# Performance work log

Measured on AMD Instinct MI355X. Metric: run time of the kernel, lower is better.

## Reference

```python
import jax, jax.numpy as jnp
import numpy as np

P = 10                      # half-window; kernel size K = 2P+1 = 21
GROUPS = ((0, 1000), (1000, 2000))  # hardcoded self.group = [0, 1000, 2000]


def setup_inputs() -> dict:
    key = jax.random.key(0)
    k1, k2, k3 = jax.random.split(key, 3)
    n, T, D = 16, 1024, 2000
    x = jax.random.normal(k1, (n, T, D), dtype=jnp.float32)
    W0 = jax.random.normal(k2, (D, 2 * P + 1), dtype=jnp.float32)
    W1 = jax.random.normal(k3, (D, 2 * P + 1), dtype=jnp.float32)
    return {"x": x, "W0": W0, "W1": W1}


def _shift_attention(x, Ws):
    n, T, D = x.shape
    K = 2 * P + 1
    # x_padded built from the ORIGINAL x under no_grad (detached)
    xp = jax.lax.stop_gradient(jnp.pad(x, ((0, 0), (P, P), (0, 0))))
    cur = x
    for Wi, (s, e) in zip(Ws, GROUPS):
        # dynamic per-timestep window weights: (n, T, K)
        w = jnp.einsum('ntd,dk->ntk', cur, Wi)
        xg = xp[:, :, s:e]  # (n, T+2P, g)
        # out[:, t, :] = sum_k w[:, t, k] * xg[:, t+k, :]  (windowed combine)
        out = w[:, :, 0, None] * xg[:, 0:T, :]
        for k in range(1, K):  # fixed small tap count, not a data-dim loop
            out = out + w[:, :, k, None] * xg[:, k:k + T, :]
        # in-place column update -> group 1 sees group 0's result in 'cur'
        cur = cur.at[:, :, s:e].set(out)
    return cur


def reference(x, W0, W1):
    return _shift_attention(x, (W0, W1))
```

## Files before the change

kernel.cpp:

```cpp
#include <hip/hip_runtime.h>

#define N_  16
#define T_  1024
#define D_  2000
#define K_  21
#define P_  10
#define NT_ (N_*T_)

__global__ void k_padW(const float* __restrict__ W0, const float* __restrict__ W1,
                       float* __restrict__ W0p, float* __restrict__ W1p) {
    int gid = blockIdx.x * blockDim.x + threadIdx.x;
    if (gid >= D_ * 24) return;
    int d = gid / 24, kk = gid - d * 24;
    W0p[gid] = (kk < K_) ? W0[d * K_ + kk] : 0.f;
    W1p[gid] = (kk < K_) ? W1[d * K_ + kk] : 0.f;
}

__global__ __launch_bounds__(256, 3)
void k_coef(const float* __restrict__ x,
            const float* __restrict__ W0p, const float* __restrict__ W1p,
            float* __restrict__ q0, float* __restrict__ q1,
            float* __restrict__ q2, float* __restrict__ q3,
            float* __restrict__ mp0, float* __restrict__ mp1,
            float* __restrict__ mp2, float* __restrict__ mp3) {
    __shared__ float lds[5888];
    const int tid  = threadIdx.x;
    const int lane = tid & 63;
    const int w    = __builtin_amdgcn_readfirstlane(tid >> 6);
    const int rg   = blockIdx.x >> 2;
    const int h    = blockIdx.x & 3;
    const int r0   = rg * 64;
    const int d0q  = h * 500;

    float a0[K_], a1[K_];
#pragma unroll
    for (int k = 0; k < K_; ++k) { a0[k] = 0.f; a1[k] = 0.f; }

    const int srow = tid >> 2;
    const int sf4  = (tid & 3) * 2;
    float4 ra, rb;

    auto load_tile = [&](int dt) {
        const int c0 = dt + sf4 * 4;
        const float* p = x + (size_t)(r0 + srow) * D_ + d0q + c0;
        ra = (c0 < 500)     ? *reinterpret_cast<const float4*>(p)
                            : make_float4(0.f, 0.f, 0.f, 0.f);
        rb = (c0 + 4 < 500) ? *reinterpret_cast<const float4*>(p + 4)
                            : make_float4(0.f, 0.f, 0.f, 0.f);
    };
    auto write_tile = [&](int buf) {
        float* b = lds + buf * 2112 + srow * 33 + sf4 * 4;
        b[0] = ra.x; b[1] = ra.y; b[2] = ra.z; b[3] = ra.w;
        b[4] = rb.x; b[5] = rb.y; b[6] = rb.z; b[7] = rb.w;
    };

    load_tile(0);
    write_tile(0);
    __syncthreads();

    for (int t = 0; t < 16; ++t) {
        if (t < 15) load_tile((t + 1) * 32);
        const int cw = (t < 15) ? 32 : 20;
        const float* xrow = lds + (t & 1) * 2112 + lane * 33;
#pragma unroll
        for (int c = 0; c < 8; ++c) {
            const int col = w * 8 + c;
            if (col < cw) {
                const int d = d0q + t * 32 + col;
                int duv;
                asm("v_mov_b32 %0, %1" : "=v"(duv) : "s"(d));
                const float* w0r = W0p + duv * 24;
                const float* w1r = W1p + duv * 24;
                float wa[21], wb[21];
#pragma unroll
                for (int j = 0; j < 5; ++j) {
                    *reinterpret_cast<float4*>(&wa[4 * j]) =
                        *reinterpret_cast<const float4*>(w0r + 4 * j);
                    *reinterpret_cast<float4*>(&wb[4 * j]) =
                        *reinterpret_cast<const float4*>(w1r + 4 * j);
                }
                wa[20] = w0r[20];
                wb[20] = w1r[20];
                const float xv = xrow[col];
#pragma unroll
                for (int k = 0; k < K_; ++k) a0[k] = fmaf(xv, wa[k], a0[k]);
#pragma unroll
                for (int k = 0; k < K_; ++k) a1[k] = fmaf(xv, wb[k], a1[k]);
            }
        }
        if (t < 15) write_tile((t + 1) & 1);
        __syncthreads();
    }

    auto reduce_store = [&](const float* acc, float* dst) {
        __syncthreads();
#pragma unroll
        for (int k = 0; k < K_; ++k) lds[tid * 23 + k] = acc[k];
        __syncthreads();
        for (int o = tid; o < 64 * K_; o += 256) {
            int tt = o / K_, j = o - tt * K_;
            float s = lds[tt * 23 + j] + lds[(64 + tt) * 23 + j] +
                      lds[(128 + tt) * 23 + j] + lds[(192 + tt) * 23 + j];
            dst[(size_t)(r0 + tt) * K_ + j] = s;
        }
    };

    float* const qd[4] = {q0, q1, q2, q3};
    float* const md[4] = {mp0, mp1, mp2, mp3};
    reduce_store(a0, qd[h]);
    reduce_store(a1, md[h]);
}

__global__ __launch_bounds__(256)
void k_finish(const float* __restrict__ q0, const float* __restrict__ q1,
              const float* __restrict__ q2, const float* __restrict__ q3,
              const float* __restrict__ mp0, const float* __restrict__ mp1,
              const float* __restrict__ mp2, const float* __restrict__ mp3,
              float* __restrict__ w0f, float* __restrict__ w1f) {
    __shared__ float w0s[64 * K_];
    __shared__ float Ms[84 * K_];
    const int tid = threadIdx.x;
    const int r0 = blockIdx.x * 64;

    for (int o = tid; o < 64 * K_; o += 256) {
        size_t g = (size_t)r0 * K_ + o;
        w0s[o] = q0[g] + q1[g] + q2[g] + q3[g];
    }
    for (int o = tid; o < 84 * K_; o += 256) {
        int i = o / K_, j = o - i * K_;
        int rr = r0 - P_ + i;
        float v = 0.f;
        if (rr >= 0 && rr < NT_) {
            size_t g = (size_t)rr * K_ + j;
            v = mp0[g] + mp1[g];
        }
        Ms[o] = v;
    }
    __syncthreads();

    for (int o = tid; o < 64 * K_; o += 256) {
        int row = o / K_, k = o - row * K_;
        size_t g = (size_t)(r0 + row) * K_ + k;
        float acc = mp2[g] + mp3[g];
        int t = (r0 + row) & (T_ - 1);
#pragma unroll
        for (int j = 0; j < K_; ++j) {
            int tt = t + j - P_;
            if (tt >= 0 && tt < T_)
                acc = fmaf(w0s[row * K_ + j], Ms[(row + j) * K_ + k], acc);
        }
        w1f[g] = acc;
        w0f[g] = w0s[o];
    }
}

__global__ __launch_bounds__(256)
void k_conv(const float* __restrict__ x, const float* __restrict__ w0f,
            const float* __restrict__ w1f, float* __restrict__ out) {
    __shared__ float xsl[84][128];
    __shared__ float wc[64 * 24];
    const int b = blockIdx.x;
    const int dseg = b & 7;
    const int tch  = (b >> 3) & 15;
    const int nn   = (b >> 7) & 15;
    const int grp  = b >> 11;
    const float* __restrict__ coef = grp ? w1f : w0f;
    const int dbase = grp * 1000;
    const int t0 = tch * 64;
    const int tid = threadIdx.x;
    const float* xb = x + (size_t)nn * T_ * D_;

    {
        const int scol = tid & 31, srow0 = tid >> 5;
#pragma unroll
        for (int pass = 0; pass < 11; ++pass) {
            int rr = srow0 + pass * 8;
            if (rr < 84) {
                int u = t0 - P_ + rr;
                int dl = dseg * 128 + scol * 4;
                float4 v = make_float4(0.f, 0.f, 0.f, 0.f);
                if (u >= 0 && u < T_ && dl < 1000)
                    v = *reinterpret_cast<const float4*>(xb + (size_t)u * D_ + dbase + dl);
                *reinterpret_cast<float4*>(&xsl[rr][scol * 4]) = v;
            }
        }
    }
    for (int o = tid; o < 64 * 24; o += 256) {
        int tl = o / 24, k = o - tl * 24;
        wc[o] = (k < K_) ? coef[((size_t)nn * T_ + t0 + tl) * K_ + k] : 0.f;
    }
    __syncthreads();

    const int wv = tid >> 6, lane = tid & 63;
    const int rw = wv * 16;
    const int dcol = dseg * 128 + lane * 2;
    const bool act = (dcol < 1000);

    float2 win[21];
#pragma unroll
    for (int s = 0; s < 21; ++s)
        win[s] = *reinterpret_cast<const float2*>(&xsl[rw + s][lane * 2]);

    float* obase = out + ((size_t)nn * T_ + t0 + rw) * D_ + dbase + dcol;

#pragma unroll
    for (int i = 0; i < 16; ++i) {
        float cfa[24];
        const float4* cf = reinterpret_cast<const float4*>(&wc[(rw + i) * 24]);
#pragma unroll
        for (int j = 0; j < 5; ++j)
            *reinterpret_cast<float4*>(&cfa[4 * j]) = cf[j];
        cfa[20] = wc[(rw + i) * 24 + 20];
        float2 acc = make_float2(0.f, 0.f);
#pragma unroll
        for (int k = 0; k < K_; ++k) {
            const float2 xv = win[(i + k) % 21];
            acc.x = fmaf(cfa[k], xv.x, acc.x);
            acc.y = fmaf(cfa[k], xv.y, acc.y);
        }
        if (act) *reinterpret_cast<float2*>(obase + (size_t)i * D_) = acc;
        if (i < 15)
            win[i % 21] = *reinterpret_cast<const float2*>(&xsl[rw + i + 21][lane * 2]);
    }
}

extern "C" void kernel_launch(void* const* d_in, const int* in_sizes, int n_in,
                              void* d_out, int out_size, void* d_ws, size_t ws_size,
                              hipStream_t stream) {
    const float* x  = (const float*)d_in[0];
    const float* W0 = (const float*)d_in[1];
    const float* W1 = (const float*)d_in[2];
    float* out = (float*)d_out;
    float* ws  = (float*)d_ws;

    const size_t CW = 344064;
    float* W0p = ws;
    float* W1p = ws + 48000;
    float* q0  = ws + 96000 + 0 * CW;
    float* q1  = ws + 96000 + 1 * CW;
    float* q2  = ws + 96000 + 2 * CW;
    float* q3  = ws + 96000 + 3 * CW;
    float* mp0 = ws + 96000 + 4 * CW;
    float* mp1 = ws + 96000 + 5 * CW;
    float* mp2 = ws + 96000 + 6 * CW;
    float* mp3 = ws + 96000 + 7 * CW;
    float* w0f = ws + 96000 + 8 * CW;
    float* w1f = ws + 96000 + 9 * CW;

    hipLaunchKernelGGL(k_padW, dim3(188), dim3(256), 0, stream, W0, W1, W0p, W1p);
    hipLaunchKernelGGL(k_coef, dim3(1024), dim3(256), 0, stream,
                       x, W0p, W1p, q0, q1, q2, q3, mp0, mp1, mp2, mp3);
    hipLaunchKernelGGL(k_finish, dim3(256), dim3(256), 0, stream,
                       q0, q1, q2, q3, mp0, mp1, mp2, mp3, w0f, w1f);
    hipLaunchKernelGGL(k_conv, dim3(4096), dim3(256), 0, stream, x, w0f, w1f, out);
}
```

Before: 438.5 us.

## Retile coefficient GEMV into 8 column slices with two rows per lane

The coefficient kernel now splits the D dimension into eight 250-wide slices over 128-row blocks. Each lane accumulates two rows, and each wave handles one weight matrix and half the columns, stored in a transposed LDS tile. This halves per-thread weight loads relative to the FMAs and removes the redundant dual-matrix loads, at the cost of eight partial buffers that the finish kernel must sum. The conv kernel also drops its LDS coefficient staging and reads coefficients directly from global memory using a wave-uniform row index.

```diff
diff --git a/kernel.cpp b/kernel.cpp
--- a/kernel.cpp
+++ b/kernel.cpp
@@ -6,6 +6,9 @@
 #define K_  21
 #define P_  10
 #define NT_ (N_*T_)
+#define SL  250
+#define RB  128
+#define PIT 129
 
 __global__ void k_padW(const float* __restrict__ W0, const float* __restrict__ W1,
                        float* __restrict__ W0p, float* __restrict__ W1p) {
@@ -16,115 +19,118 @@
     W1p[gid] = (kk < K_) ? W1[d * K_ + kk] : 0.f;
 }
 
-__global__ __launch_bounds__(256, 3)
+__global__ __launch_bounds__(256, 4)
 void k_coef(const float* __restrict__ x,
             const float* __restrict__ W0p, const float* __restrict__ W1p,
-            float* __restrict__ q0, float* __restrict__ q1,
-            float* __restrict__ q2, float* __restrict__ q3,
-            float* __restrict__ mp0, float* __restrict__ mp1,
-            float* __restrict__ mp2, float* __restrict__ mp3) {
-    __shared__ float lds[5888];
+            float* __restrict__ qb, float* __restrict__ mpb) {
+    __shared__ float lds[2 * 32 * PIT];
     const int tid  = threadIdx.x;
     const int lane = tid & 63;
     const int w    = __builtin_amdgcn_readfirstlane(tid >> 6);
-    const int rg   = blockIdx.x >> 2;
-    const int h    = blockIdx.x & 3;
-    const int r0   = rg * 64;
-    const int d0q  = h * 500;
-
-    float a0[K_], a1[K_];
-#pragma unroll
-    for (int k = 0; k < K_; ++k) { a0[k] = 0.f; a1[k] = 0.f; }
-
-    const int srow = tid >> 2;
-    const int sf4  = (tid & 3) * 2;
-    float4 ra, rb;
-
-    auto load_tile = [&](int dt) {
-        const int c0 = dt + sf4 * 4;
-        const float* p = x + (size_t)(r0 + srow) * D_ + d0q + c0;
-        ra = (c0 < 500)     ? *reinterpret_cast<const float4*>(p)
-                            : make_float4(0.f, 0.f, 0.f, 0.f);
-        rb = (c0 + 4 < 500) ? *reinterpret_cast<const float4*>(p + 4)
-                            : make_float4(0.f, 0.f, 0.f, 0.f);
+    const int rg   = blockIdx.x >> 3;
+    const int s    = blockIdx.x & 7;
+    const int r0   = rg * RB;
+    const int d0   = s * SL;
+
+    float acc[2][K_];
+#pragma unroll
+    for (int k = 0; k < K_; ++k) { acc[0][k] = 0.f; acc[1][k] = 0.f; }
+
+    const int sc2 = (tid & 15) * 2;
+    const int srw = tid >> 4;
+    float2 rv[8];
+
+    auto load_tile = [&](int ct) {
+#pragma unroll
+        for (int p = 0; p < 8; ++p) {
+            const int col = ct + sc2;
+            const float* px = x + (size_t)(r0 + srw + p * 16) * D_ + d0 + col;
+            rv[p] = (col < SL) ? *reinterpret_cast<const float2*>(px)
+                               : make_float2(0.f, 0.f);
+        }
     };
     auto write_tile = [&](int buf) {
-        float* b = lds + buf * 2112 + srow * 33 + sf4 * 4;
-        b[0] = ra.x; b[1] = ra.y; b[2] = ra.z; b[3] = ra.w;
-        b[4] = rb.x; b[5] = rb.y; b[6] = rb.z; b[7] = rb.w;
+        float* b = lds + buf * (32 * PIT);
+#pragma unroll
+        for (int p = 0; p < 8; ++p) {
+            b[sc2 * PIT + srw + p * 16]       = rv[p].x;
+            b[(sc2 + 1) * PIT + srw + p * 16] = rv[p].y;
+        }
     };
+
+    const float* __restrict__ Wsel = (w < 2) ? W0p : W1p;
+    const int cbase = (w & 1) * 16;
 
     load_tile(0);
     write_tile(0);
     __syncthreads();
 
-    for (int t = 0; t < 16; ++t) {
-        if (t < 15) load_tile((t + 1) * 32);
-        const int cw = (t < 15) ? 32 : 20;
-        const float* xrow = lds + (t & 1) * 2112 + lane * 33;
-#pragma unroll
-        for (int c = 0; c < 8; ++c) {
-            const int col = w * 8 + c;
-            if (col < cw) {
-                const int d = d0q + t * 32 + col;
-                int duv;
-                asm("v_mov_b32 %0, %1" : "=v"(duv) : "s"(d));
-                const float* w0r = W0p + duv * 24;
-                const float* w1r = W1p + duv * 24;
-                float wa[21], wb[21];
-#pragma unroll
-                for (int j = 0; j < 5; ++j) {
-                    *reinterpret_cast<float4*>(&wa[4 * j]) =
-                        *reinterpret_cast<const float4*>(w0r + 4 * j);
-                    *reinterpret_cast<float4*>(&wb[4 * j]) =
-                        *reinterpret_cast<const float4*>(w1r + 4 * j);
+    for (int t = 0; t < 8; ++t) {
+        if (t < 7) load_tile((t + 1) * 32);
+        const float* xs = lds + (t & 1) * (32 * PIT);
+        const int cw = (t < 7) ? 32 : (SL - 224);
+        int dbase;
+        asm("v_mov_b32 %0, %1" : "=v"(dbase) : "s"(d0 + t * 32));
+#pragma unroll
+        for (int c = 0; c < 16; ++c) {
+            const int cc = cbase + c;
+            if (cc < cw) {
+                const float* wr = Wsel + (size_t)(dbase + cc) * 24;
+                float wk[21];
+#pragma unroll
+                for (int j = 0; j < 5; ++j)
+                    *reinterpret_cast<float4*>(&wk[4 * j]) =
+                        *reinterpret_cast<const float4*>(wr + 4 * j);
+                wk[20] = wr[20];
+                const float2 xv =
+                    *reinterpret_cast<const float2*>(xs + cc * PIT + 2 * lane);
+#pragma unroll
+                for (int k = 0; k < K_; ++k) {
+                    acc[0][k] = fmaf(xv.x, wk[k], acc[0][k]);
+                    acc[1][k] = fmaf(xv.y, wk[k], acc[1][k]);
                 }
-                wa[20] = w0r[20];
-                wb[20] = w1r[20];
-                const float xv = xrow[col];
-#pragma unroll
-                for (int k = 0; k < K_; ++k) a0[k] = fmaf(xv, wa[k], a0[k]);
-#pragma unroll
-                for (int k = 0; k < K_; ++k) a1[k] = fmaf(xv, wb[k], a1[k]);
             }
         }
-        if (t < 15) write_tile((t + 1) & 1);
+        if (t < 7) write_tile((t + 1) & 1);
         __syncthreads();
     }
 
-    auto reduce_store = [&](const float* acc, float* dst) {
-        __syncthreads();
-#pragma unroll
-        for (int k = 0; k < K_; ++k) lds[tid * 23 + k] = acc[k];
-        __syncthreads();
-        for (int o = tid; o < 64 * K_; o += 256) {
-            int tt = o / K_, j = o - tt * K_;
-            float s = lds[tt * 23 + j] + lds[(64 + tt) * 23 + j] +
-                      lds[(128 + tt) * 23 + j] + lds[(192 + tt) * 23 + j];
-            dst[(size_t)(r0 + tt) * K_ + j] = s;
-        }
-    };
-
-    float* const qd[4] = {q0, q1, q2, q3};
-    float* const md[4] = {mp0, mp1, mp2, mp3};
-    reduce_store(a0, qd[h]);
-    reduce_store(a1, md[h]);
+    float* red = lds;
+    float* qs  = qb  + (size_t)s * (NT_ * K_);
+    float* mps = mpb + (size_t)s * (NT_ * K_);
+#define REDPASS(R)                                                              \
+    do {                                                                        \
+        __syncthreads();                                                        \
+        _Pragma("unroll")                                                       \
+        for (int k = 0; k < K_; ++k) red[tid * K_ + k] = acc[R][k];             \
+        __syncthreads();                                                        \
+        for (int o = tid; o < 64 * K_; o += 256) {                              \
+            int l = o / K_, k = o - l * K_;                                     \
+            size_t g = (size_t)(r0 + 2 * l + R) * K_ + k;                       \
+            qs[g]  = red[o] + red[o + 64 * K_];                                 \
+            mps[g] = red[o + 128 * K_] + red[o + 192 * K_];                     \
+        }                                                                       \
+    } while (0)
+    REDPASS(0);
+    REDPASS(1);
+#undef REDPASS
 }
 
 __global__ __launch_bounds__(256)
-void k_finish(const float* __restrict__ q0, const float* __restrict__ q1,
-              const float* __restrict__ q2, const float* __restrict__ q3,
-              const float* __restrict__ mp0, const float* __restrict__ mp1,
-              const float* __restrict__ mp2, const float* __restrict__ mp3,
+void k_finish(const float* __restrict__ qb, const float* __restrict__ mpb,
               float* __restrict__ w0f, float* __restrict__ w1f) {
     __shared__ float w0s[64 * K_];
     __shared__ float Ms[84 * K_];
     const int tid = threadIdx.x;
     const int r0 = blockIdx.x * 64;
+    const size_t CW = (size_t)NT_ * K_;
 
     for (int o = tid; o < 64 * K_; o += 256) {
         size_t g = (size_t)r0 * K_ + o;
-        w0s[o] = q0[g] + q1[g] + q2[g] + q3[g];
+        float v = 0.f;
+#pragma unroll
+        for (int ss = 0; ss < 8; ++ss) v += qb[ss * CW + g];
+        w0s[o] = v;
     }
     for (int o = tid; o < 84 * K_; o += 256) {
         int i = o / K_, j = o - i * K_;
@@ -132,7 +138,7 @@
         float v = 0.f;
         if (rr >= 0 && rr < NT_) {
             size_t g = (size_t)rr * K_ + j;
-            v = mp0[g] + mp1[g];
+            v = mpb[g] + mpb[CW + g] + mpb[2 * CW + g] + mpb[3 * CW + g];
         }
         Ms[o] = v;
     }
@@ -141,15 +147,16 @@
     for (int o = tid; o < 64 * K_; o += 256) {
         int row = o / K_, k = o - row * K_;
         size_t g = (size_t)(r0 + row) * K_ + k;
-        float acc = mp2[g] + mp3[g];
+        float accv = mpb[4 * CW + g] + mpb[5 * CW + g] +
+                     mpb[6 * CW + g] + mpb[7 * CW + g];
         int t = (r0 + row) & (T_ - 1);
 #pragma unroll
         for (int j = 0; j < K_; ++j) {
             int tt = t + j - P_;
             if (tt >= 0 && tt < T_)
-                acc = fmaf(w0s[row * K_ + j], Ms[(row + j) * K_ + k], acc);
-        }
-        w1f[g] = acc;
+                accv = fmaf(w0s[row * K_ + j], Ms[(row + j) * K_ + k], accv);
+        }
+        w1f[g] = accv;
         w0f[g] = w0s[o];
     }
 }
@@ -158,7 +165,6 @@
 void k_conv(const float* __restrict__ x, const float* __restrict__ w0f,
             const float* __restrict__ w1f, float* __restrict__ out) {
     __shared__ float xsl[84][128];
-    __shared__ float wc[64 * 24];
     const int b = blockIdx.x;
     const int dseg = b & 7;
     const int tch  = (b >> 3) & 15;
@@ -185,40 +191,34 @@
             }
         }
     }
-    for (int o = tid; o < 64 * 24; o += 256) {
-        int tl = o / 24, k = o - tl * 24;
-        wc[o] = (k < K_) ? coef[((size_t)nn * T_ + t0 + tl) * K_ + k] : 0.f;
-    }
     __syncthreads();
 
-    const int wv = tid >> 6, lane = tid & 63;
+    const int wv = __builtin_amdgcn_readfirstlane(tid >> 6);
+    const int lane = tid & 63;
     const int rw = wv * 16;
     const int dcol = dseg * 128 + lane * 2;
     const bool act = (dcol < 1000);
 
     float2 win[21];
 #pragma unroll
-    for (int s = 0; s < 21; ++s)
-        win[s] = *reinterpret_cast<const float2*>(&xsl[rw + s][lane * 2]);
-
+    for (int ss = 0; ss < 21; ++ss)
+        win[ss] = *reinterpret_cast<const float2*>(&xsl[rw + ss][lane * 2]);
+
+    const float* __restrict__ crow =
+        coef + ((size_t)nn * T_ + t0 + rw) * K_;
     float* obase = out + ((size_t)nn * T_ + t0 + rw) * D_ + dbase + dcol;
 
 #pragma unroll
     for (int i = 0; i < 16; ++i) {
-        float cfa[24];
-        const float4* cf = reinterpret_cast<const float4*>(&wc[(rw + i) * 24]);
-#pragma unroll
-        for (int j = 0; j < 5; ++j)
-            *reinterpret_cast<float4*>(&cfa[4 * j]) = cf[j];
-        cfa[20] = wc[(rw + i) * 24 + 20];
-        float2 acc = make_float2(0.f, 0.f);
+        float2 a2 = make_float2(0.f, 0.f);
 #pragma unroll
         for (int k = 0; k < K_; ++k) {
+            const float c = crow[i * K_ + k];
             const float2 xv = win[(i + k) % 21];
-            acc.x = fmaf(cfa[k], xv.x, acc.x);
-            acc.y = fmaf(cfa[k], xv.y, acc.y);
-        }
-        if (act) *reinterpret_cast<float2*>(obase + (size_t)i * D_) = acc;
+            a2.x = fmaf(c, xv.x, a2.x);
+            a2.y = fmaf(c, xv.y, a2.y);
+        }
+        if (act) *reinterpret_cast<float2*>(obase + (size_t)i * D_) = a2;
         if (i < 15)
             win[i % 21] = *reinterpret_cast<const float2*>(&xsl[rw + i + 21][lane * 2]);
     }
@@ -233,24 +233,18 @@
     float* out = (float*)d_out;
     float* ws  = (float*)d_ws;
 
-    const size_t CW = 344064;
+    const size_t CW = (size_t)NT_ * K_;
     float* W0p = ws;
     float* W1p = ws + 48000;
-    float* q0  = ws + 96000 + 0 * CW;
-    float* q1  = ws + 96000 + 1 * CW;
-    float* q2  = ws + 96000 + 2 * CW;
-    float* q3  = ws + 96000 + 3 * CW;
-    float* mp0 = ws + 96000 + 4 * CW;
-    float* mp1 = ws + 96000 + 5 * CW;
-    float* mp2 = ws + 96000 + 6 * CW;
-    float* mp3 = ws + 96000 + 7 * CW;
-    float* w0f = ws + 96000 + 8 * CW;
-    float* w1f = ws + 96000 + 9 * CW;
+    float* qb  = ws + 96000;
+    float* mpb = qb + 8 * CW;
+    float* w0f = mpb + 8 * CW;
+    float* w1f = w0f + CW;
 
     hipLaunchKernelGGL(k_padW, dim3(188), dim3(256), 0, stream, W0, W1, W0p, W1p);
     hipLaunchKernelGGL(k_coef, dim3(1024), dim3(256), 0, stream,
-                       x, W0p, W1p, q0, q1, q2, q3, mp0, mp1, mp2, mp3);
+                       x, W0p, W1p, qb, mpb);
     hipLaunchKernelGGL(k_finish, dim3(256), dim3(256), 0, stream,
-                       q0, q1, q2, q3, mp0, mp1, mp2, mp3, w0f, w1f);
+                       qb, mpb, w0f, w1f);
     hipLaunchKernelGGL(k_conv, dim3(4096), dim3(256), 0, stream, x, w0f, w1f, out);
 }
```

Measured after the change: 484.8 us. +10.5%, slower.
